# Kernel optimization log

Measured on AMD Instinct MI355X. Metric: run time of the kernel, lower is better.

The kernel has to match this reference:

```python
import jax, jax.numpy as jnp
import numpy as np

NUM_PAGES = 1048576
TOKENS_PER_PAGE = 32
SLOTS = 256
MAX_PAGES_PER_SLOT = 4096
MAX_SEQ = 65536  # <= max_pages_per_slot*tokens_per_page/2, leaves room to grow


def setup_inputs() -> dict:
    key = jax.random.key(0)
    k1, = jax.random.split(key, 1)
    # random current sequence lengths per slot (some may be 0 / inactive)
    seq = jax.random.randint(k1, (SLOTS,), 0, MAX_SEQ).astype(jnp.int32)
    npu = (seq + TOKENS_PER_PAGE - 1) // TOKENS_PER_PAGE  # ceil-div pages used
    cols = jnp.arange(MAX_PAGES_PER_SLOT, dtype=jnp.int32)
    # give slot i the disjoint page-id range [1 + i*2048, ...); valid since
    # max pages/slot here = ceil(65535/32) = 2048 and 1+255*2048+2047 < NUM_PAGES
    pm = jnp.where(
        cols[None, :] < npu[:, None],
        1 + jnp.arange(SLOTS, dtype=jnp.int32)[:, None] * 2048 + cols[None, :],
        -1,
    ).astype(jnp.int32)
    # mark exactly the mapped pages as in-use (index 0 used as a safe dump slot)
    safe_idx = jnp.where(pm > -1, pm, 0)
    vals = (pm > -1).astype(jnp.int32)
    page_status = jnp.zeros((NUM_PAGES,), jnp.int32).at[safe_idx].max(vals)
    page_status = page_status.at[0].set(0)
    current_page = jnp.where(
        npu > 0,
        jnp.take_along_axis(pm, jnp.maximum(npu - 1, 0)[:, None], axis=1)[:, 0],
        -1,
    ).astype(jnp.int32)
    cpp = jnp.where(seq == 0, 0, (seq - 1) % TOKENS_PER_PAGE).astype(jnp.int32)
    return {
        "page_status": page_status,
        "page_map": pm,
        "sequence_lengths": seq,
        "num_pages_used": npu.astype(jnp.int32),
        "current_page": current_page,
        "current_page_position": cpp,
    }


def _find_next_free_page(page_status):
    # matches PageManager.find_next_free_page: first free index in [1, N), else 0
    free = jnp.where(page_status[1:] == 0, size=1, fill_value=-1)[0] + 1
    return free[0].astype(jnp.int32)


def reference(page_status, page_map, sequence_lengths, num_pages_used,
              current_page, current_page_position):
    """Faithful port of PageManager.reserve_decode_step_pages (autoregressive step)."""
    tpp = TOKENS_PER_PAGE
    new_seq = sequence_lengths + jnp.where(current_page == -1, 0, 1).astype(jnp.int32)
    new_npu = (new_seq + tpp - 1) // tpp
    new_cpp = jnp.where(new_seq == 0, 0, (new_seq - 1) % tpp).astype(jnp.int32)

    def step(carry, i):
        ps, pm, cp = carry
        needs_new_page = new_npu[i] > num_pages_used[i]
        nfp = jax.lax.cond(
            needs_new_page,
            lambda: _find_next_free_page(ps),
            lambda: jnp.int32(-1),
        )
        ps = jax.lax.cond(needs_new_page, lambda x: x.at[nfp].set(1), lambda x: x, ps)
        pm = jax.lax.cond(
            needs_new_page,
            lambda x: x.at[i, num_pages_used[i]].set(nfp),
            lambda x: x,
            pm,
        )
        cp = jax.lax.cond(needs_new_page, lambda x: x.at[i].set(nfp), lambda x: x, cp)
        return (ps, pm, cp), None

    (ps, pm, cp), _ = jax.lax.scan(
        step, (page_status, page_map, current_page), jnp.arange(SLOTS, dtype=jnp.int32)
    )
    # PageState fields in declaration order
    return (ps, pm, new_seq, new_npu.astype(jnp.int32), cp, new_cpp)
```

## Files before the change

kernel.cpp:

```cpp
#include <hip/hip_runtime.h>

#define NUM_PAGES 1048576
#define TPP 32
#define SLOTS 256
#define MPPS 4096
#define NBLK 1024
#define NTHR 256

__global__ __launch_bounds__(NTHR) void fused(
    const int* __restrict__ ps, const int* __restrict__ pm,
    const int* __restrict__ seq, const int* __restrict__ npu,
    const int* __restrict__ cp, int* __restrict__ out)
{
    const int t = threadIdx.x, b = blockIdx.x;
    const int lane = t & 63, wave = t >> 6;

    int* out_ps  = out;
    int* out_pm  = out + NUM_PAGES;
    int* out_seq = out + 2 * NUM_PAGES;
    int* out_npu = out_seq + SLOTS;
    int* out_cp  = out_npu + SLOTS;
    int* out_cpp = out_cp + SLOTS;

    __shared__ int s_w[12];
    __shared__ int s_free[SLOTS];
    __shared__ int s_rank[SLOTS];
    __shared__ int s_cpo[SLOTS];
    __shared__ int s_pmval;

    const int4* ps4 = reinterpret_cast<const int4*>(ps);
    const int gi = b * NTHR + t;

    const int4 sq4 = reinterpret_cast<const int4*>(seq)[lane];
    const int4 cq4 = reinterpret_cast<const int4*>(cp)[lane];
    const int4 nu4 = reinterpret_cast<const int4*>(npu)[lane];
    const int4 pc0 = ps4[t];
    const int4 pc1 = ps4[NTHR + t];
    const int4 pc2 = ps4[2 * NTHR + t];
    int4 pv = ps4[gi];
    int4 mv = reinterpret_cast<const int4*>(pm)[gi];

    if (t == 0) s_pmval = 0;

    int ns0 = sq4.x + (cq4.x != -1), nn0 = (ns0 + TPP - 1) >> 5;
    int ns1 = sq4.y + (cq4.y != -1), nn1 = (ns1 + TPP - 1) >> 5;
    int ns2 = sq4.z + (cq4.z != -1), nn2 = (ns2 + TPP - 1) >> 5;
    int ns3 = sq4.w + (cq4.w != -1), nn3 = (ns3 + TPP - 1) >> 5;
    int nb = (nn0 > nu4.x ? 1 : 0) | (nn1 > nu4.y ? 2 : 0) |
             (nn2 > nu4.z ? 4 : 0) | (nn3 > nu4.w ? 8 : 0);
    int cnt = __popc(nb), x = cnt;
    #pragma unroll
    for (int o = 1; o < 64; o <<= 1) { int y = __shfl_up(x, o); if (lane >= o) x += y; }
    const int K = __shfl(x, 63);
    const int base_r = x - cnt;
    const int iv0 = (nb & 1) ? base_r : -1;
    const int iv1 = (nb & 2) ? base_r + (nb & 1) : -1;
    const int iv2 = (nb & 4) ? base_r + __popc(nb & 3) : -1;
    const int iv3 = (nb & 8) ? base_r + __popc(nb & 7) : -1;

    if (b == 0 && wave == 0) {
        int4 o;
        o.x = ns0; o.y = ns1; o.z = ns2; o.w = ns3;
        reinterpret_cast<int4*>(out_seq)[lane] = o;
        o.x = nn0; o.y = nn1; o.z = nn2; o.w = nn3;
        reinterpret_cast<int4*>(out_npu)[lane] = o;
        o.x = ns0 ? ((ns0 - 1) & 31) : 0;
        o.y = ns1 ? ((ns1 - 1) & 31) : 0;
        o.z = ns2 ? ((ns2 - 1) & 31) : 0;
        o.w = ns3 ? ((ns3 - 1) & 31) : 0;
        reinterpret_cast<int4*>(out_cpp)[lane] = o;
        o.x = iv0; o.y = iv1; o.z = iv2; o.w = iv3;
        reinterpret_cast<int4*>(s_rank)[lane] = o;
        reinterpret_cast<int4*>(s_cpo)[lane] = cq4;
    }

    const int slot_b = b >> 2;
    const int jb = slot_b & 3;
    int my_iv = (jb == 0) ? iv0 : (jb == 1) ? iv1 : (jb == 2) ? iv2 : iv3;
    int my_nu = (jb == 0) ? nu4.x : (jb == 1) ? nu4.y : (jb == 2) ? nu4.z : nu4.w;
    const int tr    = __shfl(my_iv, slot_b >> 2);
    const int col_b = __shfl(my_nu, slot_b >> 2);

    auto fm = [](int4 v) {
        return ((v.x == 0) ? 1 : 0) | ((v.y == 0) ? 2 : 0) |
               ((v.z == 0) ? 4 : 0) | ((v.w == 0) ? 8 : 0);
    };
    int m0 = fm(pc0), m1 = fm(pc1), m2 = fm(pc2);
    if (t == 0) m0 &= ~1;
    int q0 = __popc(m0), q1 = __popc(m1), q2 = __popc(m2);
    int x0 = q0, x1 = q1, x2 = q2;
    #pragma unroll
    for (int o = 1; o < 64; o <<= 1) {
        int y0 = __shfl_up(x0, o), y1 = __shfl_up(x1, o), y2 = __shfl_up(x2, o);
        if (lane >= o) { x0 += y0; x1 += y1; x2 += y2; }
    }
    if (lane == 63) { s_w[wave] = x0; s_w[4 + wave] = x1; s_w[8 + wave] = x2; }
    __syncthreads();
    int w0 = 0, w1 = 0, w2 = 0, T0 = 0, T1 = 0, T2 = 0;
    #pragma unroll
    for (int w = 0; w < 4; ++w) {
        int a0 = s_w[w], a1 = s_w[4 + w], a2 = s_w[8 + w];
        if (w < wave) { w0 += a0; w1 += a1; w2 += a2; }
        T0 += a0; T1 += a1; T2 += a2;
    }
    const int pos0 = w0 + x0 - q0;
    const int pos1 = T0 + w1 + x1 - q1;
    const int pos2 = T0 + T1 + w2 + x2 - q2;
    const int fe_fast = T0 + T1 + T2;

    if (b == 0) {
        #pragma unroll
        for (int j = 0; j < 4; ++j) {
            if (m0 & (1 << j)) { int p = pos0 + __popc(m0 & ((1 << j) - 1)); if (p < K) s_free[p] = t * 4 + j; }
            if (m1 & (1 << j)) { int p = pos1 + __popc(m1 & ((1 << j) - 1)); if (p < K) s_free[p] = 1024 + t * 4 + j; }
            if (m2 & (1 << j)) { int p = pos2 + __popc(m2 & ((1 << j) - 1)); if (p < K) s_free[p] = 2048 + t * 4 + j; }
        }
    }
    if (tr >= 0) {
        int fl = -1;
        #pragma unroll
        for (int j = 0; j < 4; ++j) {
            if (m0 & (1 << j)) { if (pos0 + __popc(m0 & ((1 << j) - 1)) == tr) fl = t * 4 + j; }
            if (m1 & (1 << j)) { if (pos1 + __popc(m1 & ((1 << j) - 1)) == tr) fl = 1024 + t * 4 + j; }
            if (m2 & (1 << j)) { if (pos2 + __popc(m2 & ((1 << j) - 1)) == tr) fl = 2048 + t * 4 + j; }
        }
        if (fl >= 0) s_pmval = fl;
    }

    int pmask = 0;
    if (b < 3) {
        int mm = (b == 0) ? m0 : (b == 1) ? m1 : m2;
        int pp = (b == 0) ? pos0 : (b == 1) ? pos1 : pos2;
        #pragma unroll
        for (int j = 0; j < 4; ++j)
            if (mm & (1 << j)) { int p = pp + __popc(mm & ((1 << j) - 1)); if (p < K) pmask |= 1 << j; }
    }

    int fe_total = fe_fast;
    for (int ch = 3; (ch << 10) < NUM_PAGES && fe_total < K; ++ch) {
        int4 v = ps4[(ch << 8) + t];
        int m = fm(v);
        int q = __popc(m), xx = q;
        #pragma unroll
        for (int o = 1; o < 64; o <<= 1) { int y = __shfl_up(xx, o); if (lane >= o) xx += y; }
        if (lane == 63) s_w[wave] = xx;
        __syncthreads();
        int wo = 0, T = 0;
        #pragma unroll
        for (int w = 0; w < 4; ++w) { if (w < wave) wo += s_w[w]; T += s_w[w]; }
        int pos = fe_total + wo + xx - q;
        #pragma unroll
        for (int j = 0; j < 4; ++j) if (m & (1 << j)) {
            int p = pos + __popc(m & ((1 << j) - 1));
            if (p < K) {
                int pg = (ch << 10) + (t << 2) + j;
                if (b == 0) s_free[p] = pg;
                if (p == tr) s_pmval = pg;
                if (b == ch) pmask |= 1 << j;
            }
        }
        fe_total += T;
        __syncthreads();
    }
    const int fe = (fe_total < K) ? fe_total : K;
    if (K > fe_total && gi == 0) pmask |= 1;

    __syncthreads();

    if (pmask & 1) pv.x = 1;
    if (pmask & 2) pv.y = 1;
    if (pmask & 4) pv.z = 1;
    if (pmask & 8) pv.w = 1;
    if (tr >= 0) {
        int nfp = (tr < fe) ? s_pmval : 0;
        int d = col_b - ((b & 3) << 10) - (t << 2);
        if (d == 0) mv.x = nfp;
        else if (d == 1) mv.y = nfp;
        else if (d == 2) mv.z = nfp;
        else if (d == 3) mv.w = nfp;
    }
    reinterpret_cast<int4*>(out_ps)[gi] = pv;
    reinterpret_cast<int4*>(out_pm)[gi] = mv;

    if (b == 0) {
        int rk = s_rank[t];
        out_cp[t] = (rk >= 0) ? ((rk < fe) ? s_free[rk] : 0) : s_cpo[t];
    }
}

extern "C" void kernel_launch(void* const* d_in, const int* in_sizes, int n_in,
                              void* d_out, int out_size, void* d_ws, size_t ws_size,
                              hipStream_t stream)
{
    const int* page_status = (const int*)d_in[0];
    const int* page_map    = (const int*)d_in[1];
    const int* seq         = (const int*)d_in[2];
    const int* npu         = (const int*)d_in[3];
    const int* cp          = (const int*)d_in[4];

    fused<<<NBLK, NTHR, 0, stream>>>(
        page_status, page_map, seq, npu, cp, (int*)d_out);
}
```

Before: 10.47 us.

## Halve block count and patch allocated pages with scattered writes after bulk copy

Each block now copies two int4 chunks of page_status and page_map (512 blocks instead of 1024), writing them out straight away. Every block builds the full s_free list in shared memory and afterwards patches only the allocated page_status entries and the single page_map cell that fall in its own range, using scalar scattered stores. This removes the per-element mask and page-id bookkeeping and lets the bulk copy stores issue before the scan. In exchange, every block does the shared-memory scatter work, and correctness relies on the patch stores landing after the bulk stores from the same block.

Measured after the change: 10.51 us. Within noise of the previous version (+0.4%).

```diff
diff --git a/kernel.cpp b/kernel.cpp
--- a/kernel.cpp
+++ b/kernel.cpp
@@ -4,7 +4,7 @@
 #define TPP 32
 #define SLOTS 256
 #define MPPS 4096
-#define NBLK 1024
+#define NBLK 512
 #define NTHR 256
 
 __global__ __launch_bounds__(NTHR) void fused(
@@ -26,10 +26,11 @@
     __shared__ int s_free[SLOTS];
     __shared__ int s_rank[SLOTS];
     __shared__ int s_cpo[SLOTS];
-    __shared__ int s_pmval;
 
     const int4* ps4 = reinterpret_cast<const int4*>(ps);
-    const int gi = b * NTHR + t;
+    const int4* pm4 = reinterpret_cast<const int4*>(pm);
+    const int giA = b * (2 * NTHR) + t;
+    const int giB = giA + NTHR;
 
     const int4 sq4 = reinterpret_cast<const int4*>(seq)[lane];
     const int4 cq4 = reinterpret_cast<const int4*>(cp)[lane];
@@ -37,10 +38,15 @@
     const int4 pc0 = ps4[t];
     const int4 pc1 = ps4[NTHR + t];
     const int4 pc2 = ps4[2 * NTHR + t];
-    int4 pv = ps4[gi];
-    int4 mv = reinterpret_cast<const int4*>(pm)[gi];
+    const int4 pvA = ps4[giA];
+    const int4 pvB = ps4[giB];
+    const int4 mvA = pm4[giA];
+    const int4 mvB = pm4[giB];
 
-    if (t == 0) s_pmval = 0;
+    reinterpret_cast<int4*>(out_ps)[giA] = pvA;
+    reinterpret_cast<int4*>(out_ps)[giB] = pvB;
+    reinterpret_cast<int4*>(out_pm)[giA] = mvA;
+    reinterpret_cast<int4*>(out_pm)[giB] = mvB;
 
     int ns0 = sq4.x + (cq4.x != -1), nn0 = (ns0 + TPP - 1) >> 5;
     int ns1 = sq4.y + (cq4.y != -1), nn1 = (ns1 + TPP - 1) >> 5;
@@ -74,7 +80,7 @@
         reinterpret_cast<int4*>(s_cpo)[lane] = cq4;
     }
 
-    const int slot_b = b >> 2;
+    const int slot_b = b >> 1;
     const int jb = slot_b & 3;
     int my_iv = (jb == 0) ? iv0 : (jb == 1) ? iv1 : (jb == 2) ? iv2 : iv3;
     int my_nu = (jb == 0) ? nu4.x : (jb == 1) ? nu4.y : (jb == 2) ? nu4.z : nu4.w;
@@ -106,37 +112,15 @@
     const int pos0 = w0 + x0 - q0;
     const int pos1 = T0 + w1 + x1 - q1;
     const int pos2 = T0 + T1 + w2 + x2 - q2;
-    const int fe_fast = T0 + T1 + T2;
 
-    if (b == 0) {
-        #pragma unroll
-        for (int j = 0; j < 4; ++j) {
-            if (m0 & (1 << j)) { int p = pos0 + __popc(m0 & ((1 << j) - 1)); if (p < K) s_free[p] = t * 4 + j; }
-            if (m1 & (1 << j)) { int p = pos1 + __popc(m1 & ((1 << j) - 1)); if (p < K) s_free[p] = 1024 + t * 4 + j; }
-            if (m2 & (1 << j)) { int p = pos2 + __popc(m2 & ((1 << j) - 1)); if (p < K) s_free[p] = 2048 + t * 4 + j; }
-        }
-    }
-    if (tr >= 0) {
-        int fl = -1;
-        #pragma unroll
-        for (int j = 0; j < 4; ++j) {
-            if (m0 & (1 << j)) { if (pos0 + __popc(m0 & ((1 << j) - 1)) == tr) fl = t * 4 + j; }
-            if (m1 & (1 << j)) { if (pos1 + __popc(m1 & ((1 << j) - 1)) == tr) fl = 1024 + t * 4 + j; }
-            if (m2 & (1 << j)) { if (pos2 + __popc(m2 & ((1 << j) - 1)) == tr) fl = 2048 + t * 4 + j; }
-        }
-        if (fl >= 0) s_pmval = fl;
+    #pragma unroll
+    for (int j = 0; j < 4; ++j) {
+        if (m0 & (1 << j)) { int p = pos0 + __popc(m0 & ((1 << j) - 1)); if (p < K) s_free[p] = t * 4 + j; }
+        if (m1 & (1 << j)) { int p = pos1 + __popc(m1 & ((1 << j) - 1)); if (p < K) s_free[p] = 1024 + t * 4 + j; }
+        if (m2 & (1 << j)) { int p = pos2 + __popc(m2 & ((1 << j) - 1)); if (p < K) s_free[p] = 2048 + t * 4 + j; }
     }
 
-    int pmask = 0;
-    if (b < 3) {
-        int mm = (b == 0) ? m0 : (b == 1) ? m1 : m2;
-        int pp = (b == 0) ? pos0 : (b == 1) ? pos1 : pos2;
-        #pragma unroll
-        for (int j = 0; j < 4; ++j)
-            if (mm & (1 << j)) { int p = pp + __popc(mm & ((1 << j) - 1)); if (p < K) pmask |= 1 << j; }
-    }
-
-    int fe_total = fe_fast;
+    int fe_total = T0 + T1 + T2;
     for (int ch = 3; (ch << 10) < NUM_PAGES && fe_total < K; ++ch) {
         int4 v = ps4[(ch << 8) + t];
         int m = fm(v);
@@ -152,36 +136,23 @@
         #pragma unroll
         for (int j = 0; j < 4; ++j) if (m & (1 << j)) {
             int p = pos + __popc(m & ((1 << j) - 1));
-            if (p < K) {
-                int pg = (ch << 10) + (t << 2) + j;
-                if (b == 0) s_free[p] = pg;
-                if (p == tr) s_pmval = pg;
-                if (b == ch) pmask |= 1 << j;
-            }
+            if (p < K) s_free[p] = (ch << 10) + (t << 2) + j;
         }
         fe_total += T;
         __syncthreads();
     }
     const int fe = (fe_total < K) ? fe_total : K;
-    if (K > fe_total && gi == 0) pmask |= 1;
 
     __syncthreads();
 
-    if (pmask & 1) pv.x = 1;
-    if (pmask & 2) pv.y = 1;
-    if (pmask & 4) pv.z = 1;
-    if (pmask & 8) pv.w = 1;
-    if (tr >= 0) {
-        int nfp = (tr < fe) ? s_pmval : 0;
-        int d = col_b - ((b & 3) << 10) - (t << 2);
-        if (d == 0) mv.x = nfp;
-        else if (d == 1) mv.y = nfp;
-        else if (d == 2) mv.z = nfp;
-        else if (d == 3) mv.w = nfp;
+    if (t < K) {
+        int f = (t < fe) ? s_free[t] : 0;
+        if ((f >> 11) == b) out_ps[f] = 1;
     }
-    reinterpret_cast<int4*>(out_ps)[gi] = pv;
-    reinterpret_cast<int4*>(out_pm)[gi] = mv;
-
+    if (tr >= 0 && t == 0 && ((col_b >> 11) == (b & 1))) {
+        int nfp = (tr < fe) ? s_free[tr] : 0;
+        out_pm[slot_b * MPPS + col_b] = nfp;
+    }
     if (b == 0) {
         int rk = s_rank[t];
         out_cp[t] = (rk >= 0) ? ((rk < fe) ? s_free[rk] : 0) : s_cpo[t];
```
